# Optimization experiments

Hardware: AMD Instinct MI355X
Metric: run time of the kernel (lower is better)

Reference implementation:

```python
import jax, jax.numpy as jnp
import numpy as np

D = 256; NHEAD = 8; NQ = 300; NLAYERS = 6; NLEV = 3; NPTS = 4
DFF = 1024; NCLS = 80; BS = 16
SPATIAL = ((80, 80), (40, 40), (20, 20))
LM = sum(h * w for h, w in SPATIAL)
DH = D // NHEAD
PARAM_NAMES = ['sa_wq','sa_bq','sa_wk','sa_bk','sa_wv','sa_bv','sa_wo','sa_bo',
               'ln1_g','ln1_b','ln2_g','ln2_b','ln3_g','ln3_b',
               'off_w','off_b','attw_w','attw_b','val_w','val_b','out_w','out_b',
               'ffn_w1','ffn_b1','ffn_w2','ffn_b2',
               'bb_w1','bb_b1','bb_w2','bb_b2','bb_w3','bb_b3',
               'sc_w','sc_b','qp_w1','qp_b1','qp_w2','qp_b2']


def _ln(x, g, b, eps=1e-5):
    m = x.mean(-1, keepdims=True)
    v = ((x - m) ** 2).mean(-1, keepdims=True)
    return (x - m) * jax.lax.rsqrt(v + eps) * g + b


def _mlp2(x, w1, b1, w2, b2):
    # 2-layer MLP, ReLU on hidden only (act_final_layer=False)
    return jnp.maximum(x @ w1 + b1, 0.0) @ w2 + b2


def _inv_sigmoid(x, eps=1e-5):
    x = jnp.clip(x, 0.0, 1.0)
    return jnp.log(jnp.clip(x, eps, None) / jnp.clip(1.0 - x, eps, None))


def _mha(q, k, v, wq, bq, wk, bk, wv, bv, wo, bo):
    B, N, _ = q.shape
    Q = (q @ wq + bq).reshape(B, N, NHEAD, DH)
    K = (k @ wk + bk).reshape(B, N, NHEAD, DH)
    V = (v @ wv + bv).reshape(B, N, NHEAD, DH)
    att = jnp.einsum('bqhd,bkhd->bhqk', Q, K) * (1.0 / np.sqrt(DH))
    att = jax.nn.softmax(att, axis=-1)
    o = jnp.einsum('bhqk,bkhd->bqhd', att, V).reshape(B, N, D)
    return o @ wo + bo


def _bilinear(v, x, y, Hl, Wl):
    # v: [B, Hl*Wl, C]; x, y: [B, M] pixel coords (align_corners=False, zero padding)
    x0 = jnp.floor(x); y0 = jnp.floor(y)
    wx = x - x0; wy = y - y0
    out = 0.0
    for dx, dy, w in ((0, 0, (1 - wx) * (1 - wy)), (1, 0, wx * (1 - wy)),
                      (0, 1, (1 - wx) * wy), (1, 1, wx * wy)):
        xi = x0 + dx; yi = y0 + dy
        valid = (xi >= 0) & (xi < Wl) & (yi >= 0) & (yi < Hl)
        lin = (jnp.clip(yi, 0, Hl - 1) * Wl + jnp.clip(xi, 0, Wl - 1)).astype(jnp.int32)
        g = jnp.take_along_axis(v, lin[..., None], axis=1)
        out = out + g * (w * valid)[..., None]
    return out


def _deform_attn(q, ref, memory, ow, ob, aw, ab, vw, vb, pw, pb):
    # q: [B,NQ,D]; ref: [B,NQ,4] cxcywh in [0,1]; memory: [B,LM,D]
    B = q.shape[0]
    value = (memory @ vw + vb).reshape(B, LM, NHEAD, DH)
    off = (q @ ow + ob).reshape(B, NQ, NHEAD, NLEV, NPTS, 2)
    attw = jax.nn.softmax((q @ aw + ab).reshape(B, NQ, NHEAD, NLEV * NPTS), -1)
    attw = attw.reshape(B, NQ, NHEAD, NLEV, NPTS)
    r = ref[:, :, None, None, None, :]
    loc = r[..., :2] + off / NPTS * r[..., 2:] * 0.5  # [B,NQ,H,LV,P,2]
    start = 0
    acc = 0.0
    for lv, (Hl, Wl) in enumerate(SPATIAL):
        v = value[:, start:start + Hl * Wl]  # [B, Hl*Wl, H, DH]
        v = v.transpose(0, 2, 1, 3).reshape(B * NHEAD, Hl * Wl, DH)
        g = loc[:, :, :, lv]  # [B,NQ,H,P,2]
        x = (g[..., 0] * Wl - 0.5).transpose(0, 2, 1, 3).reshape(B * NHEAD, NQ * NPTS)
        y = (g[..., 1] * Hl - 0.5).transpose(0, 2, 1, 3).reshape(B * NHEAD, NQ * NPTS)
        s = _bilinear(v, x, y, Hl, Wl).reshape(B, NHEAD, NQ, NPTS, DH)
        w = attw[:, :, :, lv].transpose(0, 2, 1, 3)  # [B,H,NQ,P]
        acc = acc + (s * w[..., None]).sum(3)  # [B,H,NQ,DH]
        start += Hl * Wl
    o = acc.transpose(0, 2, 1, 3).reshape(B, NQ, D)
    return o @ pw + pb


def _decoder(tgt, ref_points_unact, memory, p):
    ref_d = jax.nn.sigmoid(ref_points_unact)
    out = tgt
    for i in range(NLAYERS):
        pos = _mlp2(ref_d, p['qp_w1'], p['qp_b1'], p['qp_w2'], p['qp_b2'])
        q = out + pos
        t2 = _mha(q, q, out, p['sa_wq'][i], p['sa_bq'][i], p['sa_wk'][i], p['sa_bk'][i],
                  p['sa_wv'][i], p['sa_bv'][i], p['sa_wo'][i], p['sa_bo'][i])
        out = _ln(out + t2, p['ln1_g'][i], p['ln1_b'][i])
        t2 = _deform_attn(out + pos, ref_d, memory, p['off_w'][i], p['off_b'][i],
                          p['attw_w'][i], p['attw_b'][i], p['val_w'][i], p['val_b'][i],
                          p['out_w'][i], p['out_b'][i])
        out = _ln(out + t2, p['ln2_g'][i], p['ln2_b'][i])
        out = _ln(out + _mlp2(out, p['ffn_w1'][i], p['ffn_b1'][i], p['ffn_w2'][i], p['ffn_b2'][i]),
                  p['ln3_g'][i], p['ln3_b'][i])
        h = jnp.maximum(out @ p['bb_w1'][i] + p['bb_b1'][i], 0.0)
        h = jnp.maximum(h @ p['bb_w2'][i] + p['bb_b2'][i], 0.0)
        delta = h @ p['bb_w3'][i] + p['bb_b3'][i]
        ref_d = jax.nn.sigmoid(delta + _inv_sigmoid(ref_d))
    logits = out @ p['sc_w'][NLAYERS - 1] + p['sc_b'][NLAYERS - 1]
    return ref_d, logits


def setup_inputs():
    key = jax.random.key(0)
    keys = iter(jax.random.split(key, 64))
    def rn(shape, s=0.02):
        return jax.random.normal(next(keys), shape, jnp.float32) * s
    L = NLAYERS
    inp = {
        'tgt': rn((BS, NQ, D), 1.0),
        'ref_points_unact': rn((BS, NQ, 4), 1.0),
        'memory': rn((BS, LM, D), 1.0),
    }
    for n in ['sa_wq', 'sa_wk', 'sa_wv', 'sa_wo', 'val_w', 'out_w', 'bb_w1', 'bb_w2']:
        inp[n] = rn((L, D, D))
    for n in ['sa_bq', 'sa_bk', 'sa_bv', 'sa_bo', 'ln1_b', 'ln2_b', 'ln3_b',
              'val_b', 'out_b', 'ffn_b2', 'bb_b1', 'bb_b2']:
        inp[n] = jnp.zeros((L, D), jnp.float32)
    for n in ['ln1_g', 'ln2_g', 'ln3_g']:
        inp[n] = jnp.ones((L, D), jnp.float32)
    OFF = NHEAD * NLEV * NPTS * 2
    ATT = NHEAD * NLEV * NPTS
    inp['off_w'] = rn((L, D, OFF)); inp['off_b'] = rn((L, OFF), 0.1)
    inp['attw_w'] = rn((L, D, ATT)); inp['attw_b'] = jnp.zeros((L, ATT), jnp.float32)
    inp['ffn_w1'] = rn((L, D, DFF)); inp['ffn_b1'] = jnp.zeros((L, DFF), jnp.float32)
    inp['ffn_w2'] = rn((L, DFF, D))
    inp['bb_w3'] = rn((L, D, 4)); inp['bb_b3'] = jnp.zeros((L, 4), jnp.float32)
    inp['sc_w'] = rn((L, D, NCLS)); inp['sc_b'] = jnp.zeros((L, NCLS), jnp.float32)
    inp['qp_w1'] = rn((4, 2 * D)); inp['qp_b1'] = jnp.zeros((2 * D,), jnp.float32)
    inp['qp_w2'] = rn((2 * D, D)); inp['qp_b2'] = jnp.zeros((D,), jnp.float32)
    return inp


def reference(tgt, ref_points_unact, memory, sa_wq, sa_bq, sa_wk, sa_bk, sa_wv, sa_bv,
              sa_wo, sa_bo, ln1_g, ln1_b, ln2_g, ln2_b, ln3_g, ln3_b, off_w, off_b,
              attw_w, attw_b, val_w, val_b, out_w, out_b, ffn_w1, ffn_b1, ffn_w2, ffn_b2,
              bb_w1, bb_b1, bb_w2, bb_b2, bb_w3, bb_b3, sc_w, sc_b,
              qp_w1, qp_b1, qp_w2, qp_b2):
    _a = dict(locals())
    p = {k: _a[k] for k in PARAM_NAMES}
    ref_d, logits = _decoder(tgt, ref_points_unact, memory, p)
    # eval path: stacked final-layer outputs, shape [1, BS, NQ, 4] and [1, BS, NQ, NCLS]
    return ref_d[None], logits[None]
```

## Files before the change

### kernel.cpp

```cpp
#include <hip/hip_runtime.h>
#include <hip/hip_bf16.h>

typedef __hip_bfloat16 bf16;
typedef short short8 __attribute__((ext_vector_type(8)));
typedef short short4v __attribute__((ext_vector_type(4)));
typedef float float4v __attribute__((ext_vector_type(4)));

#define D_ 256
#define NHEAD_ 8
#define DH_ 32
#define NQ_ 300
#define NLAYERS_ 6
#define DFF_ 1024
#define NCLS_ 80
#define BS_ 16
#define LM_ 8400
#define BN_ (BS_*NQ_)

static __device__ __forceinline__ short f2bf(float x){
    union{float f; unsigned u;} v; v.f = x;
    unsigned r = v.u + 0x7FFF + ((v.u>>16)&1);
    return (short)(r>>16);
}
static __device__ __forceinline__ float bf2f(short s){
    union{unsigned u; float f;} v; v.u = ((unsigned)(unsigned short)s)<<16; return v.f;
}

#define LSTR 40

template<int TM, int TN, bool ABF16, bool RELU, bool OUTBF16>
__global__ __launch_bounds__(256) void mfma_gemm_kernel(
    const void* __restrict__ Av, const void* __restrict__ A2v,
    const void* __restrict__ A3v, int nA2lim,
    const short* __restrict__ WT, size_t zWT,
    const float* __restrict__ b0, const float* __restrict__ b1,
    const float* __restrict__ b2, int ns1, int ns2, size_t zB,
    void* __restrict__ Cv, size_t zC, int M, int K, int N, int nxt)
{
    __shared__ short As[2][TM*LSTR];
    __shared__ short Bs[2][TN*LSTR];
    int zz, n0;
    if(nxt){ zz = blockIdx.x / nxt; n0 = (blockIdx.x % nxt)*TN; }
    else   { zz = blockIdx.z;       n0 = blockIdx.x*TN; }
    WT += (size_t)zz*zWT; b0 += (size_t)zz*zB; b1 += (size_t)zz*zB; b2 += (size_t)zz*zB;
    int tid = threadIdx.x;
    int lane = tid&63, wave = tid>>6;
    int m0 = blockIdx.y*TM;
    const int MI = TM/32;
    const int NI = TN/32;
    int wm = (wave>>1)*(TM/2), wn = (wave&1)*(TN/2);
    int lr = lane&15, lq = lane>>4;
    float4v acc[MI][NI];
    #pragma unroll
    for(int i=0;i<MI;i++)
        #pragma unroll
        for(int j=0;j<NI;j++){ acc[i][j].x=0.f; acc[i][j].y=0.f; acc[i][j].z=0.f; acc[i][j].w=0.f; }

    const float* Af; const float* Ad; const short* Ah;
    if(ABF16){ Ah = (const short*)Av; Af=nullptr; Ad=nullptr; }
    else {
        Af = (n0 < nA2lim)? (const float*)Av : (const float*)A3v;
        Ad = (n0 < nA2lim)? (const float*)A2v : nullptr;
        Ah = nullptr;
    }

    short8  rA16[ABF16? TM/64 : 1];
    float4v rAf [ABF16? 1 : TM/32];
    float4v rAd [ABF16? 1 : TM/32];
    short8  rB[TN/64];

    auto LOAD = [&](int k0){
        if constexpr(ABF16){
            #pragma unroll
            for(int it=0; it<TM/64; ++it){
                int idx=(it*256+tid)*8; int r=idx>>5, kk=idx&31; int gm=m0+r;
                short8 v = {};
                if(gm<M) v = *(const short8*)(Ah + (size_t)gm*K + (k0+kk));
                rA16[it]=v;
            }
        } else {
            #pragma unroll
            for(int it=0; it<TM/32; ++it){
                int idx=(it*256+tid)*4; int r=idx>>5, kk=idx&31; int gm=m0+r;
                float4v v; v.x=0.f;v.y=0.f;v.z=0.f;v.w=0.f;
                float4v w; w.x=0.f;w.y=0.f;w.z=0.f;w.w=0.f;
                if(gm<M){
                    v = *(const float4v*)(Af + (size_t)gm*K + (k0+kk));
                    if(Ad) w = *(const float4v*)(Ad + (size_t)gm*K + (k0+kk));
                }
                rAf[it]=v; rAd[it]=w;
            }
        }
        #pragma unroll
        for(int it=0; it<TN/64; ++it){
            int idx=(it*256+tid)*8; int r=idx>>5, kk=idx&31; int gn=n0+r;
            short8 v = {};
            if(gn<N) v = *(const short8*)(WT + (size_t)gn*K + (k0+kk));
            rB[it]=v;
        }
    };
    auto STORE = [&](int buf){
        if constexpr(ABF16){
            #pragma unroll
            for(int it=0; it<TM/64; ++it){
                int idx=(it*256+tid)*8; int r=idx>>5, kk=idx&31;
                *(short8*)(&As[buf][r*LSTR+kk]) = rA16[it];
            }
        } else {
            #pragma unroll
            for(int it=0; it<TM/32; ++it){
                int idx=(it*256+tid)*4; int r=idx>>5, kk=idx&31;
                float4v v = rAf[it];
                if(Ad){ v.x+=rAd[it].x; v.y+=rAd[it].y; v.z+=rAd[it].z; v.w+=rAd[it].w; }
                short4v h; h.x=f2bf(v.x); h.y=f2bf(v.y); h.z=f2bf(v.z); h.w=f2bf(v.w);
                *(short4v*)(&As[buf][r*LSTR+kk]) = h;
            }
        }
        #pragma unroll
        for(int it=0; it<TN/64; ++it){
            int idx=(it*256+tid)*8; int r=idx>>5, kk=idx&31;
            *(short8*)(&Bs[buf][r*LSTR+kk]) = rB[it];
        }
    };

    const int nt = K>>5;
    LOAD(0);
    STORE(0);
    __syncthreads();
    for(int t=0; t<nt; ++t){
        int cb = t&1;
        if(t+1<nt) LOAD((t+1)<<5);
        short8 af[MI], bfr[NI];
        #pragma unroll
        for(int mi=0;mi<MI;mi++) af[mi]  = *(const short8*)(&As[cb][(wm+mi*16+lr)*LSTR + lq*8]);
        #pragma unroll
        for(int ni=0;ni<NI;ni++) bfr[ni] = *(const short8*)(&Bs[cb][(wn+ni*16+lr)*LSTR + lq*8]);
        #pragma unroll
        for(int mi=0;mi<MI;mi++)
            #pragma unroll
            for(int ni=0;ni<NI;ni++)
                acc[mi][ni] = __builtin_amdgcn_mfma_f32_16x16x32_bf16(af[mi], bfr[ni], acc[mi][ni], 0,0,0);
        if(t+1<nt){
            STORE(cb^1);
            __syncthreads();
        }
    }
    float* Cf=(float*)Cv + (size_t)zz*zC; bf16* Ch=(bf16*)Cv + (size_t)zz*zC;
    #pragma unroll
    for(int mi=0;mi<MI;mi++){
        #pragma unroll
        for(int r=0;r<4;r++){
            int gm = m0+wm+mi*16+lq*4+r;
            if(gm>=M) continue;
            #pragma unroll
            for(int ni=0;ni<NI;ni++){
                int gn = n0+wn+ni*16+lr;
                if(gn>=N) continue;
                float bv = (gn<ns1)? b0[gn] : ((gn<ns2)? b1[gn-ns1] : b2[gn-ns2]);
                float v = acc[mi][ni][r] + bv;
                if(RELU) v = fmaxf(v,0.f);
                if(OUTBF16) Ch[(size_t)gm*N+gn]=__float2bfloat16(v);
                else        Cf[(size_t)gm*N+gn]=v;
            }
        }
    }
}

__global__ __launch_bounds__(256) void fused_mha_kernel(
    const float* __restrict__ QKV, short* __restrict__ O)
{
    const int ld = 768;
    int bh = blockIdx.y; int b = bh>>3, h = bh&7;
    int q0 = blockIdx.x*64;
    __shared__ short lds[31104];
    short* Vts = lds;
    short* Qs  = lds + 10368;
    short* Ks  = lds + 12672;
    short* Ps  = lds + 10368;
    int tid = threadIdx.x;
    for(int idx=tid; idx<64*8; idx+=256){
        int r=idx>>3, c4=(idx&7)*4; int gq=q0+r;
        float4v v; v.x=0.f;v.y=0.f;v.z=0.f;v.w=0.f;
        if(gq<NQ_) v = *(const float4v*)(QKV + ((size_t)(b*NQ_+gq))*ld + h*DH_ + c4);
        short4v h4; h4.x=f2bf(v.x);h4.y=f2bf(v.y);h4.z=f2bf(v.z);h4.w=f2bf(v.w);
        *(short4v*)(Qs + r*36 + c4) = h4;
    }
    for(int idx=tid; idx<304*8; idx+=256){
        int r=idx>>3, c4=(idx&7)*4;
        float4v v; v.x=0.f;v.y=0.f;v.z=0.f;v.w=0.f;
        if(r<NQ_) v = *(const float4v*)(QKV + 256 + ((size_t)(b*NQ_+r))*ld + h*DH_ + c4);
        short4v h4; h4.x=f2bf(v.x);h4.y=f2bf(v.y);h4.z=f2bf(v.z);h4.w=f2bf(v.w);
        *(short4v*)(Ks + r*36 + c4) = h4;
    }
    for(int idx=tid; idx<320*8; idx+=256){
        int r=idx>>3, c4=(idx&7)*4;
        float4v v; v.x=0.f;v.y=0.f;v.z=0.f;v.w=0.f;
        if(r<NQ_) v = *(const float4v*)(QKV + 512 + ((size_t)(b*NQ_+r))*ld + h*DH_ + c4);
        Vts[(c4+0)*324+r]=f2bf(v.x); Vts[(c4+1)*324+r]=f2bf(v.y);
        Vts[(c4+2)*324+r]=f2bf(v.z); Vts[(c4+3)*324+r]=f2bf(v.w);
    }
    __syncthreads();

    int lane = tid&63, wave = tid>>6;
    int lr = lane&15, lq = lane>>4;
    int mrow = wave*16;
    const float scale = 0.17677669529663687f;

    float4v acc[19];
    #pragma unroll
    for(int t=0;t<19;t++){ acc[t].x=0.f; acc[t].y=0.f; acc[t].z=0.f; acc[t].w=0.f; }
    short8 afrag = *(const short8*)(&Qs[(mrow+lr)*36 + lq*8]);
    #pragma unroll
    for(int t=0;t<19;t++){
        short8 bfrag = *(const short8*)(&Ks[(t*16+lr)*36 + lq*8]);
        acc[t] = __builtin_amdgcn_mfma_f32_16x16x32_bf16(afrag, bfrag, acc[t], 0,0,0);
    }
    __syncthreads();

    for(int idx=tid; idx<64*16; idx+=256){
        int r=idx>>4, c=idx&15;
        Ps[r*324 + 304 + c]=0;
    }
    #pragma unroll
    for(int t=0;t<19;t++){
        #pragma unroll
        for(int r=0;r<4;r++) acc[t][r] *= scale;
    }
    if(lr>=12){
        #pragma unroll
        for(int r=0;r<4;r++) acc[18][r] = -1e30f;
    }
    float mx[4];
    #pragma unroll
    for(int r=0;r<4;r++){
        float m = acc[0][r];
        #pragma unroll
        for(int t=1;t<19;t++) m = fmaxf(m, acc[t][r]);
        m = fmaxf(m, __shfl_xor(m,1)); m = fmaxf(m, __shfl_xor(m,2));
        m = fmaxf(m, __shfl_xor(m,4)); m = fmaxf(m, __shfl_xor(m,8));
        mx[r]=m;
    }
    float sum[4] = {0.f,0.f,0.f,0.f};
    #pragma unroll
    for(int t=0;t<19;t++){
        #pragma unroll
        for(int r=0;r<4;r++){
            float p = __expf(acc[t][r]-mx[r]);
            acc[t][r]=p; sum[r]+=p;
        }
    }
    #pragma unroll
    for(int r=0;r<4;r++){
        float s = sum[r];
        s += __shfl_xor(s,1); s += __shfl_xor(s,2);
        s += __shfl_xor(s,4); s += __shfl_xor(s,8);
        sum[r] = 1.f/s;
    }
    #pragma unroll
    for(int t=0;t<19;t++){
        #pragma unroll
        for(int r=0;r<4;r++){
            Ps[(mrow + lq*4 + r)*324 + t*16 + lr] = f2bf(acc[t][r]*sum[r]);
        }
    }
    __syncthreads();
    float4v oacc[2];
    oacc[0].x=0.f;oacc[0].y=0.f;oacc[0].z=0.f;oacc[0].w=0.f;
    oacc[1]=oacc[0];
    #pragma unroll
    for(int kc=0;kc<10;kc++){
        short8 pa = *(const short8*)(&Ps[(mrow+lr)*324 + kc*32 + lq*8]);
        #pragma unroll
        for(int n=0;n<2;n++){
            short8 vb = *(const short8*)(&Vts[(n*16+lr)*324 + kc*32 + lq*8]);
            oacc[n] = __builtin_amdgcn_mfma_f32_16x16x32_bf16(pa, vb, oacc[n], 0,0,0);
        }
    }
    #pragma unroll
    for(int n=0;n<2;n++){
        #pragma unroll
        for(int r=0;r<4;r++){
            int gq = q0 + mrow + lq*4 + r;
            if(gq<NQ_)
                O[((size_t)(b*NQ_+gq))*D_ + h*DH_ + n*16 + lr] = f2bf(oacc[n][r]);
        }
    }
}

#define NTD 74
struct TD { const float* src; unsigned dstoff; int K, N, base; };
struct TAll { TD d[NTD]; };

__global__ __launch_bounds__(256) void transpose_all_kernel(TAll p, short* __restrict__ WTb){
    int blk = blockIdx.x;
    int di = 0;
    #pragma unroll 1
    for(int i=0;i<NTD;i++){ if(blk >= p.d[i].base) di = i; }
    TD d = p.d[di];
    int rel = blk - d.base;
    int ntx = (d.N+31)/32;
    int tn = (rel % ntx)*32, tk = (rel / ntx)*32;
    __shared__ float t[32][33];
    int tx = threadIdx.x&31, ty = threadIdx.x>>5;
    for(int i=0;i<32;i+=8){
        int k = tk+ty+i, n = tn+tx;
        t[ty+i][tx] = (k<d.K && n<d.N)? d.src[(size_t)k*d.N+n] : 0.f;
    }
    __syncthreads();
    short* out = WTb + d.dstoff;
    for(int i=0;i<32;i+=8){
        int n = tn+ty+i, k = tk+tx;
        if(n<d.N && k<d.K) out[(size_t)n*d.K+k] = f2bf(t[tx][ty+i]);
    }
}

template<bool RELU, bool BBOX>
__global__ __launch_bounds__(256) void gemm_kernel(
    const float* __restrict__ A, const float* __restrict__ W,
    const float* __restrict__ bias, float* __restrict__ Cf,
    int M, int K, int N)
{
    __shared__ float As[16][68];
    __shared__ float Bs[16][68];
    int tid = threadIdx.x;
    int m0 = blockIdx.y*64, n0 = blockIdx.x*64;
    int tm = tid>>4, tn = tid&15;
    float acc[4][4] = {};
    int lam = tid>>2;
    int lak = (tid&3)*4;
    int lbk = tid>>4;
    int lbn = (tid&15)*4;
    for(int k0=0;k0<K;k0+=16){
        {
            int m = m0+lam;
            #pragma unroll
            for(int j=0;j<4;j++){
                int k = k0+lak+j;
                float v=0.f;
                if(m<M && k<K) v = A[(size_t)m*K+k];
                As[lak+j][lam]=v;
            }
        }
        {
            int k = k0+lbk;
            #pragma unroll
            for(int j=0;j<4;j++){
                int n = n0+lbn+j;
                float v=0.f;
                if(k<K && n<N) v = W[(size_t)k*N+n];
                Bs[lbk][lbn+j]=v;
            }
        }
        __syncthreads();
        #pragma unroll
        for(int kk=0;kk<16;kk++){
            float a[4], bb[4];
            #pragma unroll
            for(int i=0;i<4;i++) a[i]=As[kk][tm*4+i];
            #pragma unroll
            for(int j=0;j<4;j++) bb[j]=Bs[kk][tn*4+j];
            #pragma unroll
            for(int i=0;i<4;i++)
                #pragma unroll
                for(int j=0;j<4;j++) acc[i][j] += a[i]*bb[j];
        }
        __syncthreads();
    }
    #pragma unroll
    for(int i=0;i<4;i++){
        int m=m0+tm*4+i; if(m>=M) continue;
        #pragma unroll
        for(int j=0;j<4;j++){
            int n=n0+tn*4+j; if(n>=N) continue;
            float v = acc[i][j] + bias[n];
            if(BBOX){
                float x = Cf[(size_t)m*N+n];
                x = fminf(fmaxf(x,0.f),1.f);
                float num = fmaxf(x,1e-5f), den = fmaxf(1.f-x,1e-5f);
                float nd = v + logf(num/den);
                Cf[(size_t)m*N+n] = 1.f/(1.f+expf(-nd));
            } else {
                if(RELU) v = fmaxf(v,0.f);
                Cf[(size_t)m*N+n]=v;
            }
        }
    }
}

__global__ void copy_kernel(const float* __restrict__ a, float* __restrict__ o, int n){
    int i = blockIdx.x*blockDim.x+threadIdx.x;
    if(i<n) o[i]=a[i];
}
__global__ void cvt_f32_bf16_kernel(const float* __restrict__ a, short* __restrict__ o, int n4){
    int i = blockIdx.x*blockDim.x+threadIdx.x;
    if(i<n4){
        float4v v = *(const float4v*)(a + (size_t)i*4);
        short4v h; h.x=f2bf(v.x); h.y=f2bf(v.y); h.z=f2bf(v.z); h.w=f2bf(v.w);
        *(short4v*)(o + (size_t)i*4) = h;
    }
}
__global__ void sigmoid_init_kernel(const float* __restrict__ a, float* __restrict__ o, int n){
    int i = blockIdx.x*blockDim.x+threadIdx.x;
    if(i<n){ float x=a[i]; o[i]=1.f/(1.f+expf(-x)); }
}
__global__ void write_out_kernel(const float* __restrict__ refd, const float* __restrict__ logits, float* __restrict__ out){
    int i = blockIdx.x*blockDim.x+threadIdx.x;
    if(i<BN_*4) out[i]=refd[i];
    else if(i<BN_*4+BN_*NCLS_) out[i]=logits[i-BN_*4];
}

__global__ __launch_bounds__(256) void ln_residual_kernel(
    float* __restrict__ cur, const short* __restrict__ t2b,
    const float* __restrict__ g, const float* __restrict__ b,
    short* __restrict__ cb)
{
    int row = blockIdx.x; int c = threadIdx.x;
    size_t idx = (size_t)row*D_+c;
    float x = cur[idx] + bf2f(t2b[idx]);
    float v1 = x, v2 = x*x;
    #pragma unroll
    for(int o=32;o>0;o>>=1){ v1 += __shfl_down(v1,o,64); v2 += __shfl_down(v2,o,64); }
    __shared__ float s1[4], s2[4], st[2];
    int wid=c>>6, lane=c&63;
    if(lane==0){ s1[wid]=v1; s2[wid]=v2; }
    __syncthreads();
    if(c==0){
        float a=0,d=0;
        #pragma unroll
        for(int i=0;i<4;i++){a+=s1[i]; d+=s2[i];}
        st[0]=a/(float)D_; st[1]=d/(float)D_;
    }
    __syncthreads();
    float m=st[0], var=st[1]-m*m;
    float y = (x-m)*rsqrtf(var+1e-5f)*g[c] + b[c];
    cur[idx]=y;
    if(cb) cb[idx]=f2bf(y);
}

__global__ __launch_bounds__(256) void deform_sample_kernel(
    const float* __restrict__ refd, const float* __restrict__ oab,
    const bf16* __restrict__ value, short* __restrict__ outacc)
{
    int row = blockIdx.x; int b = row/NQ_;
    int tid = threadIdx.x; int h = tid>>5, c = tid&31;
    __shared__ float so[192], sa[96], sr[4];
    if(tid<192) so[tid]=oab[(size_t)row*288+tid];
    if(tid<96)  sa[tid]=oab[(size_t)row*288+192+tid];
    if(tid<4)   sr[tid]=refd[(size_t)row*4+tid];
    __syncthreads();
    if(tid<8){
        float* p = sa + tid*12;
        float m=-1e30f;
        #pragma unroll
        for(int i2=0;i2<12;i2++) m=fmaxf(m,p[i2]);
        float s=0.f;
        #pragma unroll
        for(int i2=0;i2<12;i2++){ float e=__expf(p[i2]-m); p[i2]=e; s+=e; }
        float inv=1.f/s;
        #pragma unroll
        for(int i2=0;i2<12;i2++) p[i2]*=inv;
    }
    __syncthreads();
    float cx=sr[0], cy=sr[1], rw=sr[2], rh=sr[3];
    const int HS[3]={80,40,20}, WS[3]={80,40,20}, ST[3]={0,6400,8000};
    float acc=0.f;
    const bf16* vb = value + (size_t)b*LM_*D_ + h*DH_ + c;
    for(int lv=0;lv<3;lv++){
        int Hl=HS[lv], Wl=WS[lv], st=ST[lv];
        #pragma unroll
        for(int pt=0;pt<4;pt++){
            int oi = ((h*3+lv)*4+pt)*2;
            float ox=so[oi], oy=so[oi+1];
            float wa=sa[h*12+lv*4+pt];
            float lx = cx + ox*0.25f*rw*0.5f;
            float ly = cy + oy*0.25f*rh*0.5f;
            float x = lx*(float)Wl - 0.5f, y = ly*(float)Hl - 0.5f;
            float x0f=floorf(x), y0f=floorf(y);
            float wx=x-x0f, wy=y-y0f;
            int x0=(int)x0f, y0=(int)y0f;
            #pragma unroll
            for(int dy=0;dy<2;dy++){
                #pragma unroll
                for(int dx=0;dx<2;dx++){
                    int xi=x0+dx, yi=y0+dy;
                    if(xi>=0 && xi<Wl && yi>=0 && yi<Hl){
                        float w = (dx? wx : 1.f-wx)*(dy? wy : 1.f-wy);
                        int lin = yi*Wl+xi;
                        acc += __bfloat162float(vb[(size_t)(st+lin)*D_]) * (w*wa);
                    }
                }
            }
        }
    }
    outacc[(size_t)row*D_+tid]=f2bf(acc);
}

static void gemm_simt(const float*A, const float*W, const float*b, float*C,
                      int M,int K,int N, hipStream_t s, bool relu){
    dim3 g((N+63)/64,(M+63)/64);
    if(relu) gemm_kernel<true,false><<<g,256,0,s>>>(A,W,b,C,M,K,N);
    else     gemm_kernel<false,false><<<g,256,0,s>>>(A,W,b,C,M,K,N);
}
static void gemm_bbox(const float*A, const float*W, const float*b, float*refd,
                      int M,int K,int N, hipStream_t s){
    dim3 g((N+63)/64,(M+63)/64);
    gemm_kernel<false,true><<<g,256,0,s>>>(A,W,b,refd,M,K,N);
}
static void g64x(const void*A, const void*A2, const void*A3, int nA2lim,
                 const short*WT, const float*b0, const float*b1, const float*b2,
                 int ns1, int ns2, void*C, int M,int K,int N,
                 bool abf16, bool relu, bool outbf, hipStream_t s){
    dim3 g((N+63)/64,(M+63)/64,1);
    #define CALLG(AB,RL,OB) mfma_gemm_kernel<64,64,AB,RL,OB><<<g,256,0,s>>>(A,A2,A3,nA2lim,WT,0,b0,b1,b2,ns1,ns2,0,C,0,M,K,N,0)
    if(abf16){
        if(relu){ if(outbf) CALLG(true,true,true);  else CALLG(true,true,false); }
        else    { if(outbf) CALLG(true,false,true); else CALLG(true,false,false); }
    } else {
        if(relu){ if(outbf) CALLG(false,true,true);  else CALLG(false,true,false); }
        else    { if(outbf) CALLG(false,false,true); else CALLG(false,false,false); }
    }
    #undef CALLG
}
static void g64(const float*A, const float*A2, const float*A3, int nA2lim,
                const short*WT, const float*b0, const float*b1, const float*b2,
                int ns1, int ns2, void*C, int M,int K,int N,
                bool relu, bool outbf, hipStream_t s){
    g64x(A,A2,A3,nA2lim,WT,b0,b1,b2,ns1,ns2,C,M,K,N,false,relu,outbf,s);
}
static void g64b(const short*A, const short*WT, const float*b, void*C,
                 int M,int K,int N, hipStream_t s){
    g64x(A,nullptr,nullptr,1<<30,WT,b,b,b,N,N+1,C,M,K,N,true,false,true,s);
}
static int ntiles(int K,int N){ return ((N+31)/32)*((K+31)/32); }

extern "C" void kernel_launch(void* const* d_in, const int* in_sizes, int n_in,
                              void* d_out, int out_size, void* d_ws, size_t ws_size,
                              hipStream_t stream) {
    const float* tgt   = (const float*)d_in[0];
    const float* rpu   = (const float*)d_in[1];
    const float* mem   = (const float*)d_in[2];
    const float* sa_wq = (const float*)d_in[3];
    const float* sa_wk = (const float*)d_in[4];
    const float* sa_wv = (const float*)d_in[5];
    const float* sa_wo = (const float*)d_in[6];
    const float* val_w = (const float*)d_in[7];
    const float* out_w = (const float*)d_in[8];
    const float* bb_w1 = (const float*)d_in[9];
    const float* bb_w2 = (const float*)d_in[10];
    const float* sa_bq = (const float*)d_in[11];
    const float* sa_bk = (const float*)d_in[12];
    const float* sa_bv = (const float*)d_in[13];
    const float* sa_bo = (const float*)d_in[14];
    const float* ln1_b = (const float*)d_in[15];
    const float* ln2_b = (const float*)d_in[16];
    const float* ln3_b = (const float*)d_in[17];
    const float* val_b = (const float*)d_in[18];
    const float* out_b = (const float*)d_in[19];
    const float* ffn_b2= (const float*)d_in[20];
    const float* bb_b1 = (const float*)d_in[21];
    const float* bb_b2 = (const float*)d_in[22];
    const float* ln1_g = (const float*)d_in[23];
    const float* ln2_g = (const float*)d_in[24];
    const float* ln3_g = (const float*)d_in[25];
    const float* off_w = (const float*)d_in[26];
    const float* off_b = (const float*)d_in[27];
    const float* attw_w= (const float*)d_in[28];
    const float* attw_b= (const float*)d_in[29];
    const float* ffn_w1= (const float*)d_in[30];
    const float* ffn_b1= (const float*)d_in[31];
    const float* ffn_w2= (const float*)d_in[32];
    const float* bb_w3 = (const float*)d_in[33];
    const float* bb_b3 = (const float*)d_in[34];
    const float* sc_w  = (const float*)d_in[35];
    const float* sc_b  = (const float*)d_in[36];
    const float* qp_w1 = (const float*)d_in[37];
    const float* qp_b1 = (const float*)d_in[38];
    const float* qp_w2 = (const float*)d_in[39];
    const float* qp_b2 = (const float*)d_in[40];

    const size_t BND = (size_t)BN_*D_;
    const size_t USZ = (size_t)BN_*DFF_;
    const size_t LMD = (size_t)BS_*LM_*D_;
    const size_t LSZ = 1122304;

    float* ws   = (float*)d_ws;
    float* cur  = ws;
    float* pos  = cur + BND;
    float* refd = pos + BND;
    float* U    = refd + (size_t)BN_*4;
    short* tmp16 = (short*)(U + USZ);
    short* t216  = tmp16 + BND;
    short* WT    = t216 + BND;
    short* qp2T  = WT + 6*LSZ;
    short* scT   = qp2T + 131072;
    short* X     = scT + 20480;
    float* hid512 = U;
    float* QKVh   = U;
    float* offsb  = U;
    short* ffnh16 = (short*)U;
    short* bb1b   = (short*)U;
    float* bb2    = U + BND;
    float* logitsb= U;
    short* curb = tmp16;

    size_t offX = (size_t)((char*)X - (char*)d_ws);
    int vmode;
    if(ws_size >= offX + 7*LMD*2)      vmode = 3;
    else if(ws_size >= offX + 6*LMD*2) vmode = 2;
    else if(ws_size >= offX + 4*LMD)   vmode = 1;
    else                               vmode = 0;
    short* memT   = X;
    short* values = (vmode==3)? X + LMD : X;
    short* value1 = X + LMD;
    short* value0 = X;

    const int nBN_D = (int)BND;
    copy_kernel<<<(nBN_D+255)/256,256,0,stream>>>(tgt, cur, nBN_D);
    sigmoid_init_kernel<<<(BN_*4+255)/256,256,0,stream>>>(rpu, refd, BN_*4);
    if(vmode==1 || vmode==3){
        int n4 = (int)(LMD/4);
        cvt_f32_bf16_kernel<<<(n4+255)/256,256,0,stream>>>(mem, memT, n4);
    }

    {
        TAll tp; int base=0; int di=0;
        const size_t offs[12] = { 0,65536,131072,196608,262144,327680,
                                  393216,442368,466944,729088,991232,1056768 };
        const int Ks[12] = { 256,256,256,256,256,256,256,256,256,1024,256,256 };
        const int Ns[12] = { 256,256,256,256,256,256,192,96,1024,256,256,256 };
        for(int l=0;l<NLAYERS_;l++){
            const float* srcs[12] = { sa_wq+(size_t)l*D_*D_, sa_wk+(size_t)l*D_*D_, sa_wv+(size_t)l*D_*D_,
                                      sa_wo+(size_t)l*D_*D_, val_w+(size_t)l*D_*D_, out_w+(size_t)l*D_*D_,
                                      off_w+(size_t)l*D_*192, attw_w+(size_t)l*D_*96,
                                      ffn_w1+(size_t)l*D_*DFF_, ffn_w2+(size_t)l*DFF_*D_,
                                      bb_w1+(size_t)l*D_*D_, bb_w2+(size_t)l*D_*D_ };
            for(int j=0;j<12;j++){
                tp.d[di] = { srcs[j], (unsigned)(l*LSZ + offs[j]), Ks[j], Ns[j], base };
                base += ntiles(Ks[j],Ns[j]); di++;
            }
        }
        tp.d[di] = { qp_w2, (unsigned)(6*LSZ), 512, 256, base }; base += ntiles(512,256); di++;
        tp.d[di] = { sc_w + (size_t)(NLAYERS_-1)*D_*NCLS_, (unsigned)(6*LSZ+131072), 256, 80, base }; base += ntiles(256,80); di++;
        transpose_all_kernel<<<base,256,0,stream>>>(tp, WT);
    }

    if(vmode==3){
        dim3 g(12,1050,1);
        mfma_gemm_kernel<128,128,true,false,true><<<g,256,0,stream>>>(
            memT,nullptr,nullptr,1<<30, WT+262144, LSZ,
            val_b,val_b,val_b, 256,257, 256, values, LMD, BS_*LM_, D_, D_, 2);
    } else if(vmode==2){
        dim3 g(12,1050,1);
        mfma_gemm_kernel<128,128,false,false,true><<<g,256,0,stream>>>(
            mem,nullptr,mem,1<<30, WT+262144, LSZ,
            val_b,val_b,val_b, 256,257, 256, values, LMD, BS_*LM_, D_, D_, 2);
    }

    for(int i=0;i<NLAYERS_;i++){
        const bf16* value_i;
        if(vmode>=2) value_i = (const bf16*)(values + (size_t)i*LMD);
        else {
            dim3 g(2,1050,1);
            if(vmode==1){
                mfma_gemm_kernel<128,128,true,false,true><<<g,256,0,stream>>>(
                    memT,nullptr,nullptr,1<<30, WT+i*LSZ+262144, 0,
                    val_b+(size_t)i*D_,val_b,val_b, 256,257, 0, value1, 0, BS_*LM_, D_, D_, 0);
                value_i = (const bf16*)value1;
            } else {
                mfma_gemm_kernel<128,128,false,false,true><<<g,256,0,stream>>>(
                    mem,nullptr,mem,1<<30, WT+i*LSZ+262144, 0,
                    val_b+(size_t)i*D_,val_b,val_b, 256,257, 0, value0, 0, BS_*LM_, D_, D_, 0);
                value_i = (const bf16*)value0;
            }
        }
        gemm_simt(refd, qp_w1, qp_b1, hid512, BN_, 4, 512, stream, true);
        g64(hid512,nullptr,hid512,1<<30, qp2T, qp_b2,qp_b2,qp_b2, 256,257,
            pos, BN_, 512, D_, false,false, stream);
        g64(cur, pos, cur, 512, WT+i*LSZ,
            sa_bq+(size_t)i*D_, sa_bk+(size_t)i*D_, sa_bv+(size_t)i*D_, 256, 512,
            QKVh, BN_, D_, 768, false,false, stream);
        {
            dim3 g((NQ_+63)/64, BS_*NHEAD_);
            fused_mha_kernel<<<g,256,0,stream>>>(QKVh, tmp16);
        }
        g64b(tmp16, WT+i*LSZ+196608, sa_bo+(size_t)i*D_, t216, BN_, D_, D_, stream);
        ln_residual_kernel<<<BN_,256,0,stream>>>(cur, t216, ln1_g+(size_t)i*D_, ln1_b+(size_t)i*D_, nullptr);
        g64(cur, pos, cur, 1<<30, WT+i*LSZ+393216,
            off_b+(size_t)i*192, attw_b+(size_t)i*96, attw_b+(size_t)i*96, 192, 288,
            offsb, BN_, D_, 288, false,false, stream);
        deform_sample_kernel<<<BN_,256,0,stream>>>(refd, offsb, value_i, tmp16);
        g64b(tmp16, WT+i*LSZ+327680, out_b+(size_t)i*D_, t216, BN_, D_, D_, stream);
        ln_residual_kernel<<<BN_,256,0,stream>>>(cur, t216, ln2_g+(size_t)i*D_, ln2_b+(size_t)i*D_, curb);
        g64x(curb,nullptr,nullptr,1<<30, WT+i*LSZ+466944, ffn_b1+(size_t)i*DFF_,ffn_b1,ffn_b1, DFF_,DFF_+1,
             ffnh16, BN_, D_, DFF_, true,true,true, stream);
        g64x(ffnh16,nullptr,nullptr,1<<30, WT+i*LSZ+729088, ffn_b2+(size_t)i*D_,ffn_b2,ffn_b2, 256,257,
             t216, BN_, DFF_, D_, true,false,true, stream);
        ln_residual_kernel<<<BN_,256,0,stream>>>(cur, t216, ln3_g+(size_t)i*D_, ln3_b+(size_t)i*D_, curb);
        g64x(curb,nullptr,nullptr,1<<30, WT+i*LSZ+991232, bb_b1+(size_t)i*D_,bb_b1,bb_b1, 256,257,
             bb1b, BN_, D_, D_, true,true,true, stream);
        g64x(bb1b,nullptr,nullptr,1<<30, WT+i*LSZ+1056768, bb_b2+(size_t)i*D_,bb_b2,bb_b2, 256,257,
             bb2, BN_, D_, D_, true,true,false, stream);
        gemm_bbox(bb2, bb_w3+(size_t)i*D_*4, bb_b3+(size_t)i*4, refd, BN_, D_, 4, stream);
    }
    g64x(curb,nullptr,nullptr,1<<30, scT, sc_b+(size_t)(NLAYERS_-1)*NCLS_,sc_b,sc_b, NCLS_,NCLS_+1,
         logitsb, BN_, D_, NCLS_, true,false,false, stream);
    int tot = BN_*4 + BN_*NCLS_;
    write_out_kernel<<<(tot+255)/256,256,0,stream>>>(refd, logitsb, (float*)d_out);
}
```

Measured before the change: 2.426 ms.

## Add register-resident value projection kernel and fused query-pos MLP kernel

Replaces the batched 128x128 tiled value-projection GEMM with a kernel in which each block keeps a 64-row slice of memT in registers and loops over all 6 layers' weight columns, streaming weights with double buffering. Each activation row is then loaded once instead of once per layer and column tile. It also fuses the two-stage query positional MLP (the SIMT K=4 GEMM plus the MFMA GEMM) into one kernel that builds the ReLU hidden layer in shared memory. This removes the fp32 hidden-buffer round trip and one launch per layer. The costs are high register pressure in the value kernel, and uncoalesced scattered bf16 stores from the accumulator layout.

After: 2.428 ms. No clear change (+0.1%).

```diff
diff --git a/kernel.cpp b/kernel.cpp
--- a/kernel.cpp
+++ b/kernel.cpp
@@ -24,6 +24,135 @@
 }
 static __device__ __forceinline__ float bf2f(short s){
     union{unsigned u; float f;} v; v.u = ((unsigned)(unsigned short)s)<<16; return v.f;
+}
+
+__global__ __launch_bounds__(256) void valproj_kernel(
+    const short* __restrict__ memT, const short* __restrict__ WTall, size_t zWT,
+    const float* __restrict__ vb, short* __restrict__ values)
+{
+    int m0 = blockIdx.x*64;
+    int tid = threadIdx.x, lane = tid&63, wave = tid>>6;
+    int wm = (wave>>1)*32, wn = (wave&1)*32;
+    int lr = lane&15, lq = lane>>4;
+    short8 af[2][8];
+    #pragma unroll
+    for(int t=0;t<8;t++){
+        #pragma unroll
+        for(int mi=0;mi<2;mi++)
+            af[mi][t] = *(const short8*)(memT + (size_t)(m0+wm+mi*16+lr)*256 + t*32 + lq*8);
+    }
+    short8 pb[2][2];
+    #pragma unroll
+    for(int ni=0;ni<2;ni++)
+        pb[0][ni] = *(const short8*)(WTall + (size_t)(wn+ni*16+lr)*256 + lq*8);
+    for(int c=0;c<24;c++){
+        int zi = c>>2;
+        int n0 = (c&3)*64;
+        float4v acc[2][2];
+        #pragma unroll
+        for(int i=0;i<2;i++)
+            #pragma unroll
+            for(int j=0;j<2;j++){ acc[i][j].x=0.f; acc[i][j].y=0.f; acc[i][j].z=0.f; acc[i][j].w=0.f; }
+        const short* wz = WTall + (size_t)zi*zWT;
+        #pragma unroll
+        for(int t=0;t<8;t++){
+            const int cur = t&1;
+            if(t<7){
+                #pragma unroll
+                for(int ni=0;ni<2;ni++)
+                    pb[cur^1][ni] = *(const short8*)(wz + (size_t)(n0+wn+ni*16+lr)*256 + (t+1)*32 + lq*8);
+            } else if(c<23){
+                int c2 = c+1; int zi2 = c2>>2; int n02 = (c2&3)*64;
+                const short* wz2 = WTall + (size_t)zi2*zWT;
+                #pragma unroll
+                for(int ni=0;ni<2;ni++)
+                    pb[cur^1][ni] = *(const short8*)(wz2 + (size_t)(n02+wn+ni*16+lr)*256 + lq*8);
+            }
+            acc[0][0] = __builtin_amdgcn_mfma_f32_16x16x32_bf16(af[0][t], pb[cur][0], acc[0][0], 0,0,0);
+            acc[0][1] = __builtin_amdgcn_mfma_f32_16x16x32_bf16(af[0][t], pb[cur][1], acc[0][1], 0,0,0);
+            acc[1][0] = __builtin_amdgcn_mfma_f32_16x16x32_bf16(af[1][t], pb[cur][0], acc[1][0], 0,0,0);
+            acc[1][1] = __builtin_amdgcn_mfma_f32_16x16x32_bf16(af[1][t], pb[cur][1], acc[1][1], 0,0,0);
+        }
+        const float* bb = vb + (size_t)zi*256;
+        bf16* out = (bf16*)values + (size_t)zi*((size_t)134400*256);
+        #pragma unroll
+        for(int mi=0;mi<2;mi++){
+            #pragma unroll
+            for(int rr=0;rr<4;rr++){
+                int gm = m0+wm+mi*16+lq*4+rr;
+                #pragma unroll
+                for(int ni=0;ni<2;ni++){
+                    int gn = n0+wn+ni*16+lr;
+                    out[(size_t)gm*256+gn] = __float2bfloat16(acc[mi][ni][rr]+bb[gn]);
+                }
+            }
+        }
+    }
+}
+
+__global__ __launch_bounds__(256) void pos_mlp_kernel(
+    const float* __restrict__ refd, const float* __restrict__ w1, const float* __restrict__ b1,
+    const short* __restrict__ w2T, const float* __restrict__ b2, float* __restrict__ pos)
+{
+    __shared__ short hs[32*520];
+    __shared__ float rs[32*4];
+    int n0 = blockIdx.x*64, m0 = blockIdx.y*32;
+    int tid = threadIdx.x;
+    if(tid<128) rs[tid] = refd[(size_t)m0*4 + tid];
+    __syncthreads();
+    {
+        int c0 = tid&255;
+        float w1r[2][4], b1r[2];
+        #pragma unroll
+        for(int h=0;h<2;h++){
+            int c = c0 + h*256;
+            b1r[h] = b1[c];
+            #pragma unroll
+            for(int k=0;k<4;k++) w1r[h][k] = w1[k*512+c];
+        }
+        #pragma unroll 4
+        for(int j=0;j<64;j++){
+            int r = j>>1, h = j&1;
+            int c = c0 + h*256;
+            float v = 0.f;
+            #pragma unroll
+            for(int k=0;k<4;k++) v = fmaf(rs[r*4+k], w1r[h][k], v);
+            v += b1r[h];
+            hs[r*520+c] = f2bf(fmaxf(v,0.f));
+        }
+    }
+    __syncthreads();
+    int lane = tid&63, wave = tid>>6;
+    int wm = (wave>>1)*16, wn = (wave&1)*32;
+    int lr = lane&15, lq = lane>>4;
+    float4v acc[2];
+    #pragma unroll
+    for(int j=0;j<2;j++){ acc[j].x=0.f; acc[j].y=0.f; acc[j].z=0.f; acc[j].w=0.f; }
+    short8 pb[2][2];
+    #pragma unroll
+    for(int ni=0;ni<2;ni++)
+        pb[0][ni] = *(const short8*)(w2T + (size_t)(n0+wn+ni*16+lr)*512 + lq*8);
+    #pragma unroll
+    for(int t=0;t<16;t++){
+        const int cur = t&1;
+        if(t<15){
+            #pragma unroll
+            for(int ni=0;ni<2;ni++)
+                pb[cur^1][ni] = *(const short8*)(w2T + (size_t)(n0+wn+ni*16+lr)*512 + (t+1)*32 + lq*8);
+        }
+        short8 a0 = *(const short8*)(&hs[(wm+lr)*520 + t*32 + lq*8]);
+        acc[0] = __builtin_amdgcn_mfma_f32_16x16x32_bf16(a0, pb[cur][0], acc[0], 0,0,0);
+        acc[1] = __builtin_amdgcn_mfma_f32_16x16x32_bf16(a0, pb[cur][1], acc[1], 0,0,0);
+    }
+    #pragma unroll
+    for(int rr=0;rr<4;rr++){
+        int gm = m0+wm+lq*4+rr;
+        #pragma unroll
+        for(int ni=0;ni<2;ni++){
+            int gn = n0+wn+ni*16+lr;
+            pos[(size_t)gm*256+gn] = acc[ni][rr] + b2[gn];
+        }
+    }
 }
 
 #define LSTR 40
@@ -495,12 +624,6 @@
     outacc[(size_t)row*D_+tid]=f2bf(acc);
 }
 
-static void gemm_simt(const float*A, const float*W, const float*b, float*C,
-                      int M,int K,int N, hipStream_t s, bool relu){
-    dim3 g((N+63)/64,(M+63)/64);
-    if(relu) gemm_kernel<true,false><<<g,256,0,s>>>(A,W,b,C,M,K,N);
-    else     gemm_kernel<false,false><<<g,256,0,s>>>(A,W,b,C,M,K,N);
-}
 static void gemm_bbox(const float*A, const float*W, const float*b, float*refd,
                       int M,int K,int N, hipStream_t s){
     dim3 g((N+63)/64,(M+63)/64);
@@ -594,7 +717,6 @@
     short* qp2T  = WT + 6*LSZ;
     short* scT   = qp2T + 131072;
     short* X     = scT + 20480;
-    float* hid512 = U;
     float* QKVh   = U;
     float* offsb  = U;
     short* ffnh16 = (short*)U;
@@ -645,10 +767,7 @@
     }
 
     if(vmode==3){
-        dim3 g(12,1050,1);
-        mfma_gemm_kernel<128,128,true,false,true><<<g,256,0,stream>>>(
-            memT,nullptr,nullptr,1<<30, WT+262144, LSZ,
-            val_b,val_b,val_b, 256,257, 256, values, LMD, BS_*LM_, D_, D_, 2);
+        valproj_kernel<<<2100,256,0,stream>>>(memT, WT+262144, LSZ, val_b, values);
     } else if(vmode==2){
         dim3 g(12,1050,1);
         mfma_gemm_kernel<128,128,false,false,true><<<g,256,0,stream>>>(
@@ -673,9 +792,7 @@
                 value_i = (const bf16*)value0;
             }
         }
-        gemm_simt(refd, qp_w1, qp_b1, hid512, BN_, 4, 512, stream, true);
-        g64(hid512,nullptr,hid512,1<<30, qp2T, qp_b2,qp_b2,qp_b2, 256,257,
-            pos, BN_, 512, D_, false,false, stream);
+        pos_mlp_kernel<<<dim3(4,150),256,0,stream>>>(refd, qp_w1, qp_b1, qp2T, qp_b2, pos);
         g64(cur, pos, cur, 512, WT+i*LSZ,
             sa_bq+(size_t)i*D_, sa_bk+(size_t)i*D_, sa_bv+(size_t)i*D_, 256, 512,
             QKVh, BN_, D_, 768, false,false, stream);
```
